# Performance work log

Measured on AMD Instinct MI355X. Metric: run time of the kernel, lower is better.

## Reference

```python
import jax, jax.numpy as jnp
import numpy as np

N_NODES = 50000
N_EDGES = 800000
NUM_RELATIONS = 8   # 2 * n_speakers**2 with n_speakers = 2
NUM_BASES = 30
G_DIM, H1_DIM, H2_DIM = 128, 128, 128


def setup_inputs() -> dict:
    key = jax.random.key(0)
    ks = jax.random.split(key, 10)
    inp = {
        "node_features": jax.random.normal(ks[0], (N_NODES, G_DIM), jnp.float32),
        "edge_index": jax.random.randint(ks[1], (2, N_EDGES), 0, N_NODES, dtype=jnp.int64),
        "edge_type": jax.random.randint(ks[2], (N_EDGES,), 0, NUM_RELATIONS, dtype=jnp.int64),
        "edge_norm": jax.random.uniform(ks[3], (N_EDGES,), jnp.float32),
        # RGCNConv params (basis decomposition)
        "basis": jax.random.normal(ks[4], (NUM_BASES, G_DIM, H1_DIM), jnp.float32) * 0.05,
        "comp": jax.random.normal(ks[5], (NUM_RELATIONS, NUM_BASES), jnp.float32) * 0.1,
        "root": jax.random.normal(ks[6], (G_DIM, H1_DIM), jnp.float32) * 0.05,
        "bias1": jnp.zeros((H1_DIM,), jnp.float32),
        # GraphConv params: lin_rel (with bias) applied to aggregated neighbors, lin_root (no bias)
        "w_rel": jax.random.normal(ks[7], (H1_DIM, H2_DIM), jnp.float32) * 0.05,
        "b_rel": jnp.zeros((H2_DIM,), jnp.float32),
        "w_root": jax.random.normal(ks[8], (H1_DIM, H2_DIM), jnp.float32) * 0.05,
    }
    return inp


def reference(node_features, edge_index, edge_type, edge_norm,
              basis, comp, root, bias1, w_rel, b_rel, w_root):
    src, dst = edge_index[0], edge_index[1]  # source_to_target flow (PyG default)

    # ---- Layer 1: RGCNConv with basis decomposition ----
    # W[r] = sum_b comp[r,b] * basis[b]  -> [R, g, h1]
    W = jnp.einsum('rb,bio->rio', comp, basis)
    # Project every node under every relation once (N*R*h1), then gather per edge.
    # Mathematically identical to per-edge x_j @ W[edge_type] but avoids an [E, g, h1] tensor.
    x_proj = jnp.einsum('ni,rio->nro', node_features, W)  # [N, R, h1]
    msg = x_proj[src, edge_type] * edge_norm[:, None]     # [E, h1]
    agg = jax.ops.segment_sum(msg, dst, num_segments=N_NODES)  # scatter-add to targets
    h = agg + node_features @ root + bias1                # [N, h1]

    # ---- Layer 2: GraphConv (aggr='add', no edge_weight) ----
    agg2 = jax.ops.segment_sum(h[src], dst, num_segments=N_NODES)  # [N, h1]
    out = agg2 @ w_rel + b_rel + h @ w_root               # [N, h2]
    return out
```

## Files before the change

kernel.cpp:

```cpp
#include <hip/hip_runtime.h>
#include <hip/hip_bf16.h>
#include <stdint.h>

#define N_NODES 50000
#define N_EDGES 800000
#define NREL    8
#define NBASES  30
#define DIM     128
#define NSLOT   9
#define NCAT    (NSLOT*DIM)
#define SCAN_NB ((N_NODES + 255) / 256)
#define NB_C    196
#define EPB_PLACE 2048
#define NBLK_PLACE ((N_EDGES + EPB_PLACE - 1) / EPB_PLACE)
#define GEMM1_TILES ((N_NODES + 63) / 64)
#define PREP_TOTAL  (NCAT * DIM + 2 * DIM * DIM)
#define PREP_BLKS   ((PREP_TOTAL + 255) / 256)
#define CONV_BLKS   ((N_NODES * DIM / 4 + 255) / 256)
#define HIST_BLKS   ((N_EDGES + 255) / 256)

typedef __attribute__((ext_vector_type(8))) short short8;
typedef __attribute__((ext_vector_type(4))) float floatx4;
typedef __hip_bfloat16  bf16;
typedef __hip_bfloat162 bf16x2;

__device__ inline ushort f2bu(float f) { bf16 b = __float2bfloat16(f); return *(ushort*)&b; }
__device__ inline float  bu2f(ushort u) { union { unsigned i; float f; } c; c.i = ((unsigned)u) << 16; return c.f; }

__global__ __launch_bounds__(256) void setup_kernel(const float* __restrict__ basis, const float* __restrict__ comp,
                                                    const float* __restrict__ root, const float* __restrict__ w_rel,
                                                    const float* __restrict__ w_root,
                                                    bf16* __restrict__ WcatT, bf16* __restrict__ wrelT,
                                                    bf16* __restrict__ wrootT,
                                                    const float4* __restrict__ x4, ushort4* __restrict__ xb4,
                                                    const int* __restrict__ ei, int* __restrict__ deg) {
    int b = blockIdx.x;
    if (b < PREP_BLKS) {
        int idx = b * 256 + threadIdx.x;
        const int n_cat = NCAT * DIM;
        const int n_sq  = DIM * DIM;
        if (idx < n_cat) {
            int k = idx & 127, n = idx >> 7;
            int r = n >> 7, o = n & 127;
            float v;
            if (r < NREL) {
                v = 0.f;
                for (int bb = 0; bb < NBASES; ++bb)
                    v += comp[r * NBASES + bb] * basis[(bb * DIM + k) * DIM + o];
            } else {
                v = root[k * DIM + o];
            }
            WcatT[n * DIM + k] = __float2bfloat16(v);
        } else if (idx < n_cat + n_sq) {
            int t = idx - n_cat; int k = t & 127, o = t >> 7;
            wrelT[o * DIM + k] = __float2bfloat16(w_rel[k * DIM + o]);
        } else if (idx < n_cat + 2 * n_sq) {
            int t = idx - n_cat - n_sq; int k = t & 127, o = t >> 7;
            wrootT[o * DIM + k] = __float2bfloat16(w_root[k * DIM + o]);
        }
    } else if (b < PREP_BLKS + CONV_BLKS) {
        int i = (b - PREP_BLKS) * 256 + threadIdx.x;
        int n4 = N_NODES * DIM / 4;
        if (i < n4) {
            float4 f = x4[i];
            ushort4 o;
            o.x = f2bu(f.x); o.y = f2bu(f.y); o.z = f2bu(f.z); o.w = f2bu(f.w);
            xb4[i] = o;
        }
    } else {
        int e = (b - PREP_BLKS - CONV_BLKS) * 256 + threadIdx.x;
        if (e < N_EDGES) atomicAdd(&deg[ei[N_EDGES + e]], 1);
    }
}

__global__ __launch_bounds__(256) void scan_one(const int* __restrict__ deg, int* __restrict__ segoff,
                                                unsigned long long* __restrict__ bstate, int n) {
    __shared__ int buf[256];
    int b = blockIdx.x, tid = threadIdx.x;
    int i = b * 256 + tid;
    int v = (i < n) ? deg[i] : 0;
    buf[tid] = v;
    __syncthreads();
#pragma unroll
    for (int o = 1; o < 256; o <<= 1) {
        int t = (tid >= o) ? buf[tid - o] : 0;
        __syncthreads();
        buf[tid] += t;
        __syncthreads();
    }
    int incl = buf[tid];
    int total = buf[255];
    if (tid == 0)
        __hip_atomic_store(&bstate[b], (1ULL << 32) | (unsigned)total,
                           __ATOMIC_RELEASE, __HIP_MEMORY_SCOPE_AGENT);
    int mysum = 0;
    for (int j = tid; j < b; j += 256) {
        unsigned long long s;
        do {
            s = __hip_atomic_load(&bstate[j], __ATOMIC_ACQUIRE, __HIP_MEMORY_SCOPE_AGENT);
        } while (!(s >> 32));
        mysum += (int)(s & 0xFFFFFFFFu);
    }
    __syncthreads();
    buf[tid] = mysum;
    __syncthreads();
#pragma unroll
    for (int o = 128; o > 0; o >>= 1) {
        if (tid < o) buf[tid] += buf[tid + o];
        __syncthreads();
    }
    int base = buf[0];
    if (i < n) segoff[i + 1] = base + incl;
    if (b == 0 && tid == 0) segoff[0] = 0;
}

__global__ __launch_bounds__(256) void gemm1_place(const bf16* __restrict__ A, const bf16* __restrict__ BT,
                                                   bf16* __restrict__ C, int M,
                                                   const int* __restrict__ ei, const int* __restrict__ et,
                                                   const float* __restrict__ en, const int* __restrict__ segoff,
                                                   int* __restrict__ bcur, uint2* __restrict__ tmp) {
    __shared__ ushort smem[2 * 64 * 136];
    int blk = blockIdx.x;
    if (blk < GEMM1_TILES) {
        ushort (*As)[136] = (ushort(*)[136])smem;
        ushort (*Bs)[136] = (ushort(*)[136])(smem + 64 * 136);
        const ushort* Au = (const ushort*)A;
        const ushort* Bu = (const ushort*)BT;
        ushort* Cu = (ushort*)C;
        int tm = blk * 64;
        int wave = threadIdx.x >> 6, lane = threadIdx.x & 63;
        int q = lane >> 4, mr = lane & 15;

#pragma unroll
        for (int u = 0; u < 4; ++u) {
            int cc = threadIdx.x + u * 256;
            int row = cc >> 4, seg = cc & 15;
            int gr = tm + row;
            short8 av = {0, 0, 0, 0, 0, 0, 0, 0};
            if (gr < M) av = *(const short8*)(Au + (size_t)gr * 128 + seg * 8);
            *(short8*)(&As[row][seg * 8]) = av;
        }

        floatx4 zero = {0.f, 0.f, 0.f, 0.f};
        for (int t = 0; t < 18; ++t) {
            if (t) __syncthreads();
#pragma unroll
            for (int u = 0; u < 4; ++u) {
                int cc = threadIdx.x + u * 256;
                int row = cc >> 4, seg = cc & 15;
                short8 bv = *(const short8*)(Bu + (size_t)(t * 64 + row) * 128 + seg * 8);
                *(short8*)(&Bs[row][seg * 8]) = bv;
            }
            __syncthreads();
            floatx4 acc[4] = {zero, zero, zero, zero};
#pragma unroll
            for (int kt = 0; kt < 4; ++kt) {
                short8 a = *(const short8*)(&As[wave * 16 + mr][q * 8 + kt * 32]);
#pragma unroll
                for (int nt = 0; nt < 4; ++nt) {
                    short8 bb = *(const short8*)(&Bs[nt * 16 + mr][q * 8 + kt * 32]);
                    acc[nt] = __builtin_amdgcn_mfma_f32_16x16x32_bf16(a, bb, acc[nt], 0, 0, 0);
                }
            }
#pragma unroll
            for (int nt = 0; nt < 4; ++nt)
#pragma unroll
                for (int r4 = 0; r4 < 4; ++r4) {
                    int row = tm + wave * 16 + q * 4 + r4;
                    if (row < M) Cu[(size_t)row * NCAT + t * 64 + nt * 16 + mr] = f2bu(acc[nt][r4]);
                }
        }
    } else {
        int* lhist = (int*)smem;
        int* lbase = lhist + NB_C;
        int* lrank = lbase + NB_C;
        int tid = threadIdx.x;
        for (int i = tid; i < NB_C; i += 256) { lhist[i] = 0; lrank[i] = 0; }
        __syncthreads();
        int e0 = (blk - GEMM1_TILES) * EPB_PLACE;
#pragma unroll
        for (int i = 0; i < EPB_PLACE / 256; ++i) {
            int e = e0 + i * 256 + tid;
            if (e < N_EDGES) atomicAdd(&lhist[ei[N_EDGES + e] >> 8], 1);
        }
        __syncthreads();
        for (int c = tid; c < NB_C; c += 256)
            if (lhist[c] > 0) lbase[c] = atomicAdd(&bcur[c], lhist[c]);
        __syncthreads();
#pragma unroll
        for (int i = 0; i < EPB_PLACE / 256; ++i) {
            int e = e0 + i * 256 + tid;
            if (e < N_EDGES) {
                int d = ei[N_EDGES + e];
                int c = d >> 8;
                int r = atomicAdd(&lrank[c], 1);
                int p = segoff[c << 8] + lbase[c] + r;
                tmp[p] = make_uint2((unsigned)ei[e] | ((unsigned)et[e] << 16) | ((unsigned)(d & 255) << 19),
                                    __float_as_uint(en[e]));
            }
        }
    }
}

__global__ __launch_bounds__(256) void sortb_kernel(const uint2* __restrict__ tmp, const int* __restrict__ segoff,
                                                    uint2* __restrict__ rec) {
    __shared__ int cur[256];
    int c = blockIdx.x;
    int tid = threadIdx.x;
    cur[tid] = 0;
    __syncthreads();
    int base = segoff[c << 8];
    int nlimit = (c + 1) << 8; if (nlimit > N_NODES) nlimit = N_NODES;
    int end = segoff[nlimit];
    for (int i = base + tid; i < end; i += 256) {
        uint2 r = tmp[i];
        int dl = (r.x >> 19) & 255;
        int p = segoff[(c << 8) + dl] + atomicAdd(&cur[dl], 1);
        rec[p] = make_uint2(r.x & 0x7FFFFu, r.y);
    }
}

__global__ void seg1_kernel(const uint2* __restrict__ rec, const int* __restrict__ segoff,
                            const ushort* __restrict__ proj, const float* __restrict__ bias1,
                            ushort* __restrict__ h) {
    int quad = threadIdx.x >> 4;
    int node = blockIdx.x * 16 + quad;
    if (node >= N_NODES) return;
    int lane = threadIdx.x & 15;
    int s = segoff[node], e = segoff[node + 1];
    float acc[8] = {0.f, 0.f, 0.f, 0.f, 0.f, 0.f, 0.f, 0.f};
    for (int chunk = s; chunk < e; chunk += 4) {
        int m = e - chunk; if (m > 4) m = 4;
        uint2 rr[4]; short8 vv[4];
#pragma unroll
        for (int j = 0; j < 4; ++j) if (j < m) rr[j] = rec[chunk + j];
#pragma unroll
        for (int j = 0; j < 4; ++j) if (j < m) {
            unsigned src = rr[j].x & 0xFFFFu;
            unsigned typ = rr[j].x >> 16;
            vv[j] = *(const short8*)(proj + ((size_t)src * NSLOT + typ) * 128 + lane * 8);
        }
#pragma unroll
        for (int j = 0; j < 4; ++j) if (j < m) {
            float norm = __uint_as_float(rr[j].y);
#pragma unroll
            for (int f = 0; f < 8; ++f) acc[f] += norm * bu2f((ushort)vv[j][f]);
        }
    }
    short8 base = *(const short8*)(proj + ((size_t)node * NSLOT + 8) * 128 + lane * 8);
    short8 o;
#pragma unroll
    for (int f = 0; f < 8; ++f)
        o[f] = (short)f2bu(acc[f] + bu2f((ushort)base[f]) + bias1[lane * 8 + f]);
    *(short8*)(h + (size_t)node * 128 + lane * 8) = o;
}

__global__ void seg2_kernel(const uint2* __restrict__ rec, const int* __restrict__ segoff,
                            const ushort* __restrict__ h, ushort* __restrict__ out2) {
    int quad = threadIdx.x >> 4;
    int node = blockIdx.x * 16 + quad;
    if (node >= N_NODES) return;
    int lane = threadIdx.x & 15;
    int s = segoff[node], e = segoff[node + 1];
    float acc[8] = {0.f, 0.f, 0.f, 0.f, 0.f, 0.f, 0.f, 0.f};
    for (int chunk = s; chunk < e; chunk += 4) {
        int m = e - chunk; if (m > 4) m = 4;
        uint2 rr[4]; short8 vv[4];
#pragma unroll
        for (int j = 0; j < 4; ++j) if (j < m) rr[j] = rec[chunk + j];
#pragma unroll
        for (int j = 0; j < 4; ++j) if (j < m)
            vv[j] = *(const short8*)(h + (size_t)(rr[j].x & 0xFFFFu) * 128 + lane * 8);
#pragma unroll
        for (int j = 0; j < 4; ++j) if (j < m)
#pragma unroll
            for (int f = 0; f < 8; ++f) acc[f] += bu2f((ushort)vv[j][f]);
    }
    short8 o;
#pragma unroll
    for (int f = 0; f < 8; ++f) o[f] = (short)f2bu(acc[f]);
    *(short8*)(out2 + (size_t)node * 128 + lane * 8) = o;
}

__global__ __launch_bounds__(256) void gemm2_kernel(const bf16* __restrict__ A1, const bf16* __restrict__ B1T,
                                                    const bf16* __restrict__ A2, const bf16* __restrict__ B2T,
                                                    const float* __restrict__ brel, float* __restrict__ out, int M) {
    __shared__ ushort As[64][136];
    __shared__ ushort Bs[64][136];
    int tm = blockIdx.x * 64, tn = blockIdx.y * 64;
    int wave = threadIdx.x >> 6, lane = threadIdx.x & 63;
    int q = lane >> 4, mr = lane & 15;
    floatx4 zero = {0.f, 0.f, 0.f, 0.f};
    floatx4 acc[4] = {zero, zero, zero, zero};

    for (int phase = 0; phase < 2; ++phase) {
        const ushort* Au = (const ushort*)(phase ? A2 : A1);
        const ushort* Bu = (const ushort*)(phase ? B2T : B1T);
        if (phase) __syncthreads();
        for (int c = threadIdx.x; c < 64 * 16; c += 256) {
            int row = c >> 4, seg = c & 15;
            int gr = tm + row;
            short8 av = {0, 0, 0, 0, 0, 0, 0, 0};
            if (gr < M) av = *(const short8*)(Au + (size_t)gr * 128 + seg * 8);
            *(short8*)(&As[row][seg * 8]) = av;
            short8 bv = *(const short8*)(Bu + (size_t)(tn + row) * 128 + seg * 8);
            *(short8*)(&Bs[row][seg * 8]) = bv;
        }
        __syncthreads();
#pragma unroll
        for (int kt = 0; kt < 4; ++kt) {
            short8 a = *(const short8*)(&As[wave * 16 + mr][q * 8 + kt * 32]);
#pragma unroll
            for (int nt = 0; nt < 4; ++nt) {
                short8 b = *(const short8*)(&Bs[nt * 16 + mr][q * 8 + kt * 32]);
                acc[nt] = __builtin_amdgcn_mfma_f32_16x16x32_bf16(a, b, acc[nt], 0, 0, 0);
            }
        }
    }
    __syncthreads();
    float* Csf = (float*)&As[0][0];
#pragma unroll
    for (int nt = 0; nt < 4; ++nt)
#pragma unroll
        for (int r4 = 0; r4 < 4; ++r4) {
            int row = wave * 16 + q * 4 + r4;
            int col = nt * 16 + mr;
            Csf[row * 68 + col] = acc[nt][r4] + brel[tn + col];
        }
    __syncthreads();
#pragma unroll
    for (int u = 0; u < 4; ++u) {
        int cc = threadIdx.x + u * 256;
        int row = cc >> 4, seg = cc & 15;
        int gr = tm + row;
        if (gr < M) {
            float4 v = *(const float4*)(&Csf[row * 68 + seg * 4]);
            *(float4*)(out + (size_t)gr * 128 + tn + seg * 4) = v;
        }
    }
}

extern "C" void kernel_launch(void* const* d_in, const int* in_sizes, int n_in,
                              void* d_out, int out_size, void* d_ws, size_t ws_size,
                              hipStream_t stream) {
    const float* x      = (const float*)d_in[0];
    const int*   ei     = (const int*)d_in[1];
    const int*   et     = (const int*)d_in[2];
    const float* en     = (const float*)d_in[3];
    const float* basis  = (const float*)d_in[4];
    const float* comp   = (const float*)d_in[5];
    const float* root   = (const float*)d_in[6];
    const float* bias1  = (const float*)d_in[7];
    const float* w_rel  = (const float*)d_in[8];
    const float* b_rel  = (const float*)d_in[9];
    const float* w_root = (const float*)d_in[10];
    float* out = (float*)d_out;

    char* ws = (char*)d_ws;
    size_t off = 0;
    auto alloc = [&](size_t bytes) { size_t o = off; off += (bytes + 255) & ~(size_t)255; return o; };

    size_t o_deg    = alloc((size_t)N_NODES * 4);
    size_t o_bcur   = alloc((size_t)NB_C * 4);
    size_t o_bstate = alloc((size_t)SCAN_NB * 8);
    size_t o_segoff = alloc((size_t)(N_NODES + 1) * 4);
    size_t o_rec    = alloc((size_t)N_EDGES * 8);
    size_t o_tmp    = alloc((size_t)N_EDGES * 8);
    size_t o_wcat   = alloc((size_t)NCAT * DIM * 2);
    size_t o_wrel   = alloc((size_t)DIM * DIM * 2);
    size_t o_wroot  = alloc((size_t)DIM * DIM * 2);
    size_t o_xb     = alloc((size_t)N_NODES * DIM * 2);
    size_t o_proj   = alloc((size_t)N_NODES * NCAT * 2);
    size_t o_hb     = alloc((size_t)N_NODES * DIM * 2);
    size_t o_agg2   = alloc((size_t)N_NODES * DIM * 2);

    int*   deg    = (int*)(ws + o_deg);
    int*   bcur   = (int*)(ws + o_bcur);
    unsigned long long* bstate = (unsigned long long*)(ws + o_bstate);
    int*   segoff = (int*)(ws + o_segoff);
    uint2* rec    = (uint2*)(ws + o_rec);
    uint2* tmp    = (uint2*)(ws + o_tmp);
    bf16*  wcat   = (bf16*)(ws + o_wcat);
    bf16*  wrelT  = (bf16*)(ws + o_wrel);
    bf16*  wrootT = (bf16*)(ws + o_wroot);
    bf16*  xb     = (bf16*)(ws + o_xb);
    bf16*  proj   = (bf16*)(ws + o_proj);
    bf16*  hb     = (bf16*)(ws + o_hb);
    bf16*  agg2   = (bf16*)(ws + o_agg2);

    hipMemsetAsync(ws + o_deg, 0, o_segoff - o_deg, stream);

    setup_kernel<<<PREP_BLKS + CONV_BLKS + HIST_BLKS, 256, 0, stream>>>(
        basis, comp, root, w_rel, w_root, wcat, wrelT, wrootT,
        (const float4*)x, (ushort4*)xb, ei, deg);
    scan_one<<<SCAN_NB, 256, 0, stream>>>(deg, segoff, bstate, N_NODES);
    gemm1_place<<<GEMM1_TILES + NBLK_PLACE, 256, 0, stream>>>(xb, wcat, proj, N_NODES,
                                                              ei, et, en, segoff, bcur, tmp);
    sortb_kernel<<<NB_C, 256, 0, stream>>>(tmp, segoff, rec);
    seg1_kernel<<<(N_NODES + 15) / 16, 256, 0, stream>>>(rec, segoff, (const ushort*)proj, bias1, (ushort*)hb);
    seg2_kernel<<<(N_NODES + 15) / 16, 256, 0, stream>>>(rec, segoff, (const ushort*)hb, (ushort*)agg2);
    {
        dim3 grid((N_NODES + 63) / 64, DIM / 64);
        gemm2_kernel<<<grid, 256, 0, stream>>>(agg2, wrelT, hb, wrootT, b_rel, out, N_NODES);
    }
}
```

Baseline: 320.8 us.

## Aggregate raw features per relation before projecting, replacing project-then-gather

Measured after the change: 350.5 us. 1.09x slower.

```diff
diff --git a/kernel.cpp b/kernel.cpp
--- a/kernel.cpp
+++ b/kernel.cpp
@@ -13,7 +13,7 @@
 #define NB_C    196
 #define EPB_PLACE 2048
 #define NBLK_PLACE ((N_EDGES + EPB_PLACE - 1) / EPB_PLACE)
-#define GEMM1_TILES ((N_NODES + 63) / 64)
+#define GEMMH_TILES ((N_NODES + 63) / 64)
 #define PREP_TOTAL  (NCAT * DIM + 2 * DIM * DIM)
 #define PREP_BLKS   ((PREP_TOTAL + 255) / 256)
 #define CONV_BLKS   ((N_NODES * DIM / 4 + 255) / 256)
@@ -30,7 +30,7 @@
 __global__ __launch_bounds__(256) void setup_kernel(const float* __restrict__ basis, const float* __restrict__ comp,
                                                     const float* __restrict__ root, const float* __restrict__ w_rel,
                                                     const float* __restrict__ w_root,
-                                                    bf16* __restrict__ WcatT, bf16* __restrict__ wrelT,
+                                                    bf16* __restrict__ W2T, bf16* __restrict__ wrelT,
                                                     bf16* __restrict__ wrootT,
                                                     const float4* __restrict__ x4, ushort4* __restrict__ xb4,
                                                     const int* __restrict__ ei, int* __restrict__ deg) {
@@ -40,8 +40,9 @@
         const int n_cat = NCAT * DIM;
         const int n_sq  = DIM * DIM;
         if (idx < n_cat) {
-            int k = idx & 127, n = idx >> 7;
-            int r = n >> 7, o = n & 127;
+            int o = idx / NCAT;
+            int rem = idx - o * NCAT;
+            int r = rem >> 7, k = rem & 127;
             float v;
             if (r < NREL) {
                 v = 0.f;
@@ -50,7 +51,7 @@
             } else {
                 v = root[k * DIM + o];
             }
-            WcatT[n * DIM + k] = __float2bfloat16(v);
+            W2T[idx] = __float2bfloat16(v);
         } else if (idx < n_cat + n_sq) {
             int t = idx - n_cat; int k = t & 127, o = t >> 7;
             wrelT[o * DIM + k] = __float2bfloat16(w_rel[k * DIM + o]);
@@ -114,145 +115,174 @@
     if (b == 0 && tid == 0) segoff[0] = 0;
 }
 
-__global__ __launch_bounds__(256) void gemm1_place(const bf16* __restrict__ A, const bf16* __restrict__ BT,
-                                                   bf16* __restrict__ C, int M,
-                                                   const int* __restrict__ ei, const int* __restrict__ et,
-                                                   const float* __restrict__ en, const int* __restrict__ segoff,
-                                                   int* __restrict__ bcur, uint2* __restrict__ tmp) {
-    __shared__ ushort smem[2 * 64 * 136];
-    int blk = blockIdx.x;
-    if (blk < GEMM1_TILES) {
-        ushort (*As)[136] = (ushort(*)[136])smem;
-        ushort (*Bs)[136] = (ushort(*)[136])(smem + 64 * 136);
-        const ushort* Au = (const ushort*)A;
-        const ushort* Bu = (const ushort*)BT;
-        ushort* Cu = (ushort*)C;
-        int tm = blk * 64;
-        int wave = threadIdx.x >> 6, lane = threadIdx.x & 63;
-        int q = lane >> 4, mr = lane & 15;
-
+__global__ __launch_bounds__(256) void place_kernel(const int* __restrict__ ei, const int* __restrict__ et,
+                                                    const float* __restrict__ en, const int* __restrict__ segoff,
+                                                    int* __restrict__ bcur, uint2* __restrict__ tmp) {
+    __shared__ int lhist[NB_C];
+    __shared__ int lbase[NB_C];
+    __shared__ int lrank[NB_C];
+    int tid = threadIdx.x;
+    for (int i = tid; i < NB_C; i += 256) { lhist[i] = 0; lrank[i] = 0; }
+    __syncthreads();
+    int e0 = blockIdx.x * EPB_PLACE;
+#pragma unroll
+    for (int i = 0; i < EPB_PLACE / 256; ++i) {
+        int e = e0 + i * 256 + tid;
+        if (e < N_EDGES) atomicAdd(&lhist[ei[N_EDGES + e] >> 8], 1);
+    }
+    __syncthreads();
+    for (int c = tid; c < NB_C; c += 256)
+        if (lhist[c] > 0) lbase[c] = atomicAdd(&bcur[c], lhist[c]);
+    __syncthreads();
+#pragma unroll
+    for (int i = 0; i < EPB_PLACE / 256; ++i) {
+        int e = e0 + i * 256 + tid;
+        if (e < N_EDGES) {
+            int d = ei[N_EDGES + e];
+            int c = d >> 8;
+            int r = atomicAdd(&lrank[c], 1);
+            int p = segoff[c << 8] + lbase[c] + r;
+            tmp[p] = make_uint2((unsigned)ei[e] | ((unsigned)et[e] << 16) | ((unsigned)(d & 255) << 19),
+                                __float_as_uint(en[e]));
+        }
+    }
+}
+
+__global__ __launch_bounds__(256) void sortb_kernel(const uint2* __restrict__ tmp, const int* __restrict__ segoff,
+                                                    uint2* __restrict__ rec) {
+    __shared__ int hist2[256 * 8];
+    int c = blockIdx.x;
+    int tid = threadIdx.x;
+    for (int i = tid; i < 256 * 8; i += 256) hist2[i] = 0;
+    __syncthreads();
+    int base = segoff[c << 8];
+    int nlimit = (c + 1) << 8; if (nlimit > N_NODES) nlimit = N_NODES;
+    int end = segoff[nlimit];
+    for (int i = base + tid; i < end; i += 256) {
+        unsigned x = tmp[i].x;
+        int dl = (x >> 19) & 255, ty = (x >> 16) & 7;
+        atomicAdd(&hist2[dl * 8 + ty], 1);
+    }
+    __syncthreads();
+    {
+        int node = (c << 8) + tid;
+        int run = (node < N_NODES) ? (segoff[node] - base) : 0;
+#pragma unroll
+        for (int t = 0; t < 8; ++t) {
+            int cnt = hist2[tid * 8 + t];
+            hist2[tid * 8 + t] = run;
+            run += cnt;
+        }
+    }
+    __syncthreads();
+    for (int i = base + tid; i < end; i += 256) {
+        uint2 r = tmp[i];
+        int dl = (r.x >> 19) & 255, ty = (r.x >> 16) & 7;
+        int p = base + atomicAdd(&hist2[dl * 8 + ty], 1);
+        rec[p] = make_uint2(r.x & 0x7FFFFu, r.y);
+    }
+}
+
+__device__ inline void flush8(ushort* dst, const float* acc) {
+    short8 o;
+#pragma unroll
+    for (int f = 0; f < 8; ++f) o[f] = (short)f2bu(acc[f]);
+    *(short8*)dst = o;
+}
+
+__global__ void gath1_kernel(const uint2* __restrict__ rec, const int* __restrict__ segoff,
+                             const ushort* __restrict__ xb, ushort* __restrict__ s) {
+    int quad = threadIdx.x >> 4;
+    int node = blockIdx.x * 16 + quad;
+    if (node >= N_NODES) return;
+    int lane = threadIdx.x & 15;
+    ushort* sp = s + (size_t)node * NCAT + lane * 8;
+    int st = segoff[node], en = segoff[node + 1];
+    float acc[8] = {0.f, 0.f, 0.f, 0.f, 0.f, 0.f, 0.f, 0.f};
+    int cur = -1;
+    unsigned mask = 0;
+    for (int chunk = st; chunk < en; chunk += 4) {
+        int m = en - chunk; if (m > 4) m = 4;
+        uint2 rr[4]; short8 vv[4];
+#pragma unroll
+        for (int j = 0; j < 4; ++j) if (j < m) rr[j] = rec[chunk + j];
+#pragma unroll
+        for (int j = 0; j < 4; ++j) if (j < m)
+            vv[j] = *(const short8*)(xb + (size_t)(rr[j].x & 0xFFFFu) * 128 + lane * 8);
+#pragma unroll
+        for (int j = 0; j < 4; ++j) if (j < m) {
+            int ty = (int)(rr[j].x >> 16);
+            if (ty != cur) {
+                if (cur >= 0) flush8(sp + cur * 128, acc);
+                cur = ty;
+                mask |= 1u << ty;
+#pragma unroll
+                for (int f = 0; f < 8; ++f) acc[f] = 0.f;
+            }
+            float nrm = __uint_as_float(rr[j].y);
+#pragma unroll
+            for (int f = 0; f < 8; ++f) acc[f] += nrm * bu2f((ushort)vv[j][f]);
+        }
+    }
+    if (cur >= 0) flush8(sp + cur * 128, acc);
+    short8 z = {0, 0, 0, 0, 0, 0, 0, 0};
+#pragma unroll
+    for (int t = 0; t < 8; ++t)
+        if (!(mask & (1u << t))) *(short8*)(sp + t * 128) = z;
+    *(short8*)(sp + 8 * 128) = *(const short8*)(xb + (size_t)node * 128 + lane * 8);
+}
+
+__global__ __launch_bounds__(256) void gemmh_kernel(const bf16* __restrict__ S, const bf16* __restrict__ B2T,
+                                                    const float* __restrict__ bias1, bf16* __restrict__ H, int M) {
+    __shared__ ushort As[64][136];
+    __shared__ ushort Bs[128][136];
+    const ushort* Su = (const ushort*)S;
+    const ushort* Bu = (const ushort*)B2T;
+    ushort* Hu = (ushort*)H;
+    int tm = blockIdx.x * 64;
+    int wave = threadIdx.x >> 6, lane = threadIdx.x & 63;
+    int q = lane >> 4, mr = lane & 15;
+    floatx4 zero = {0.f, 0.f, 0.f, 0.f};
+    floatx4 acc[8] = {zero, zero, zero, zero, zero, zero, zero, zero};
+
+    for (int ch = 0; ch < 9; ++ch) {
+        if (ch) __syncthreads();
 #pragma unroll
         for (int u = 0; u < 4; ++u) {
             int cc = threadIdx.x + u * 256;
             int row = cc >> 4, seg = cc & 15;
             int gr = tm + row;
             short8 av = {0, 0, 0, 0, 0, 0, 0, 0};
-            if (gr < M) av = *(const short8*)(Au + (size_t)gr * 128 + seg * 8);
+            if (gr < M) av = *(const short8*)(Su + (size_t)gr * NCAT + ch * 128 + seg * 8);
             *(short8*)(&As[row][seg * 8]) = av;
         }
-
-        floatx4 zero = {0.f, 0.f, 0.f, 0.f};
-        for (int t = 0; t < 18; ++t) {
-            if (t) __syncthreads();
-#pragma unroll
-            for (int u = 0; u < 4; ++u) {
-                int cc = threadIdx.x + u * 256;
-                int row = cc >> 4, seg = cc & 15;
-                short8 bv = *(const short8*)(Bu + (size_t)(t * 64 + row) * 128 + seg * 8);
-                *(short8*)(&Bs[row][seg * 8]) = bv;
+#pragma unroll
+        for (int u = 0; u < 8; ++u) {
+            int cc = threadIdx.x + u * 256;
+            int row = cc >> 4, seg = cc & 15;
+            short8 bv = *(const short8*)(Bu + (size_t)row * NCAT + ch * 128 + seg * 8);
+            *(short8*)(&Bs[row][seg * 8]) = bv;
+        }
+        __syncthreads();
+#pragma unroll
+        for (int kt = 0; kt < 4; ++kt) {
+            short8 a = *(const short8*)(&As[wave * 16 + mr][q * 8 + kt * 32]);
+#pragma unroll
+            for (int nt = 0; nt < 8; ++nt) {
+                short8 b = *(const short8*)(&Bs[nt * 16 + mr][q * 8 + kt * 32]);
+                acc[nt] = __builtin_amdgcn_mfma_f32_16x16x32_bf16(a, b, acc[nt], 0, 0, 0);
             }
-            __syncthreads();
-            floatx4 acc[4] = {zero, zero, zero, zero};
-#pragma unroll
-            for (int kt = 0; kt < 4; ++kt) {
-                short8 a = *(const short8*)(&As[wave * 16 + mr][q * 8 + kt * 32]);
-#pragma unroll
-                for (int nt = 0; nt < 4; ++nt) {
-                    short8 bb = *(const short8*)(&Bs[nt * 16 + mr][q * 8 + kt * 32]);
-                    acc[nt] = __builtin_amdgcn_mfma_f32_16x16x32_bf16(a, bb, acc[nt], 0, 0, 0);
-                }
-            }
-#pragma unroll
-            for (int nt = 0; nt < 4; ++nt)
-#pragma unroll
-                for (int r4 = 0; r4 < 4; ++r4) {
-                    int row = tm + wave * 16 + q * 4 + r4;
-                    if (row < M) Cu[(size_t)row * NCAT + t * 64 + nt * 16 + mr] = f2bu(acc[nt][r4]);
-                }
-        }
-    } else {
-        int* lhist = (int*)smem;
-        int* lbase = lhist + NB_C;
-        int* lrank = lbase + NB_C;
-        int tid = threadIdx.x;
-        for (int i = tid; i < NB_C; i += 256) { lhist[i] = 0; lrank[i] = 0; }
-        __syncthreads();
-        int e0 = (blk - GEMM1_TILES) * EPB_PLACE;
-#pragma unroll
-        for (int i = 0; i < EPB_PLACE / 256; ++i) {
-            int e = e0 + i * 256 + tid;
-            if (e < N_EDGES) atomicAdd(&lhist[ei[N_EDGES + e] >> 8], 1);
-        }
-        __syncthreads();
-        for (int c = tid; c < NB_C; c += 256)
-            if (lhist[c] > 0) lbase[c] = atomicAdd(&bcur[c], lhist[c]);
-        __syncthreads();
-#pragma unroll
-        for (int i = 0; i < EPB_PLACE / 256; ++i) {
-            int e = e0 + i * 256 + tid;
-            if (e < N_EDGES) {
-                int d = ei[N_EDGES + e];
-                int c = d >> 8;
-                int r = atomicAdd(&lrank[c], 1);
-                int p = segoff[c << 8] + lbase[c] + r;
-                tmp[p] = make_uint2((unsigned)ei[e] | ((unsigned)et[e] << 16) | ((unsigned)(d & 255) << 19),
-                                    __float_as_uint(en[e]));
-            }
-        }
-    }
-}
-
-__global__ __launch_bounds__(256) void sortb_kernel(const uint2* __restrict__ tmp, const int* __restrict__ segoff,
-                                                    uint2* __restrict__ rec) {
-    __shared__ int cur[256];
-    int c = blockIdx.x;
-    int tid = threadIdx.x;
-    cur[tid] = 0;
-    __syncthreads();
-    int base = segoff[c << 8];
-    int nlimit = (c + 1) << 8; if (nlimit > N_NODES) nlimit = N_NODES;
-    int end = segoff[nlimit];
-    for (int i = base + tid; i < end; i += 256) {
-        uint2 r = tmp[i];
-        int dl = (r.x >> 19) & 255;
-        int p = segoff[(c << 8) + dl] + atomicAdd(&cur[dl], 1);
-        rec[p] = make_uint2(r.x & 0x7FFFFu, r.y);
-    }
-}
-
-__global__ void seg1_kernel(const uint2* __restrict__ rec, const int* __restrict__ segoff,
-                            const ushort* __restrict__ proj, const float* __restrict__ bias1,
-                            ushort* __restrict__ h) {
-    int quad = threadIdx.x >> 4;
-    int node = blockIdx.x * 16 + quad;
-    if (node >= N_NODES) return;
-    int lane = threadIdx.x & 15;
-    int s = segoff[node], e = segoff[node + 1];
-    float acc[8] = {0.f, 0.f, 0.f, 0.f, 0.f, 0.f, 0.f, 0.f};
-    for (int chunk = s; chunk < e; chunk += 4) {
-        int m = e - chunk; if (m > 4) m = 4;
-        uint2 rr[4]; short8 vv[4];
-#pragma unroll
-        for (int j = 0; j < 4; ++j) if (j < m) rr[j] = rec[chunk + j];
-#pragma unroll
-        for (int j = 0; j < 4; ++j) if (j < m) {
-            unsigned src = rr[j].x & 0xFFFFu;
-            unsigned typ = rr[j].x >> 16;
-            vv[j] = *(const short8*)(proj + ((size_t)src * NSLOT + typ) * 128 + lane * 8);
-        }
-#pragma unroll
-        for (int j = 0; j < 4; ++j) if (j < m) {
-            float norm = __uint_as_float(rr[j].y);
-#pragma unroll
-            for (int f = 0; f < 8; ++f) acc[f] += norm * bu2f((ushort)vv[j][f]);
-        }
-    }
-    short8 base = *(const short8*)(proj + ((size_t)node * NSLOT + 8) * 128 + lane * 8);
-    short8 o;
-#pragma unroll
-    for (int f = 0; f < 8; ++f)
-        o[f] = (short)f2bu(acc[f] + bu2f((ushort)base[f]) + bias1[lane * 8 + f]);
-    *(short8*)(h + (size_t)node * 128 + lane * 8) = o;
+        }
+    }
+#pragma unroll
+    for (int nt = 0; nt < 8; ++nt) {
+        float bi = bias1[nt * 16 + mr];
+#pragma unroll
+        for (int r4 = 0; r4 < 4; ++r4) {
+            int row = tm + wave * 16 + q * 4 + r4;
+            if (row < M) Hu[(size_t)row * 128 + nt * 16 + mr] = f2bu(acc[nt][r4] + bi);
+        }
+    }
 }
 
 __global__ void seg2_kernel(const uint2* __restrict__ rec, const int* __restrict__ segoff,
@@ -261,10 +291,10 @@
     int node = blockIdx.x * 16 + quad;
     if (node >= N_NODES) return;
     int lane = threadIdx.x & 15;
-    int s = segoff[node], e = segoff[node + 1];
+    int st = segoff[node], en = segoff[node + 1];
     float acc[8] = {0.f, 0.f, 0.f, 0.f, 0.f, 0.f, 0.f, 0.f};
-    for (int chunk = s; chunk < e; chunk += 4) {
-        int m = e - chunk; if (m > 4) m = 4;
+    for (int chunk = st; chunk < en; chunk += 4) {
+        int m = en - chunk; if (m > 4) m = 4;
         uint2 rr[4]; short8 vv[4];
 #pragma unroll
         for (int j = 0; j < 4; ++j) if (j < m) rr[j] = rec[chunk + j];
@@ -366,11 +396,11 @@
     size_t o_segoff = alloc((size_t)(N_NODES + 1) * 4);
     size_t o_rec    = alloc((size_t)N_EDGES * 8);
     size_t o_tmp    = alloc((size_t)N_EDGES * 8);
-    size_t o_wcat   = alloc((size_t)NCAT * DIM * 2);
+    size_t o_w2t    = alloc((size_t)NCAT * DIM * 2);
     size_t o_wrel   = alloc((size_t)DIM * DIM * 2);
     size_t o_wroot  = alloc((size_t)DIM * DIM * 2);
     size_t o_xb     = alloc((size_t)N_NODES * DIM * 2);
-    size_t o_proj   = alloc((size_t)N_NODES * NCAT * 2);
+    size_t o_s      = alloc((size_t)N_NODES * NCAT * 2);
     size_t o_hb     = alloc((size_t)N_NODES * DIM * 2);
     size_t o_agg2   = alloc((size_t)N_NODES * DIM * 2);
 
@@ -380,24 +410,24 @@
     int*   segoff = (int*)(ws + o_segoff);
     uint2* rec    = (uint2*)(ws + o_rec);
     uint2* tmp    = (uint2*)(ws + o_tmp);
-    bf16*  wcat   = (bf16*)(ws + o_wcat);
+    bf16*  w2t    = (bf16*)(ws + o_w2t);
     bf16*  wrelT  = (bf16*)(ws + o_wrel);
     bf16*  wrootT = (bf16*)(ws + o_wroot);
     bf16*  xb     = (bf16*)(ws + o_xb);
-    bf16*  proj   = (bf16*)(ws + o_proj);
+    bf16*  sbuf   = (bf16*)(ws + o_s);
     bf16*  hb     = (bf16*)(ws + o_hb);
     bf16*  agg2   = (bf16*)(ws + o_agg2);
 
     hipMemsetAsync(ws + o_deg, 0, o_segoff - o_deg, stream);
 
     setup_kernel<<<PREP_BLKS + CONV_BLKS + HIST_BLKS, 256, 0, stream>>>(
-        basis, comp, root, w_rel, w_root, wcat, wrelT, wrootT,
+        basis, comp, root, w_rel, w_root, w2t, wrelT, wrootT,
         (const float4*)x, (ushort4*)xb, ei, deg);
     scan_one<<<SCAN_NB, 256, 0, stream>>>(deg, segoff, bstate, N_NODES);
-    gemm1_place<<<GEMM1_TILES + NBLK_PLACE, 256, 0, stream>>>(xb, wcat, proj, N_NODES,
-                                                              ei, et, en, segoff, bcur, tmp);
+    place_kernel<<<NBLK_PLACE, 256, 0, stream>>>(ei, et, en, segoff, bcur, tmp);
     sortb_kernel<<<NB_C, 256, 0, stream>>>(tmp, segoff, rec);
-    seg1_kernel<<<(N_NODES + 15) / 16, 256, 0, stream>>>(rec, segoff, (const ushort*)proj, bias1, (ushort*)hb);
+    gath1_kernel<<<(N_NODES + 15) / 16, 256, 0, stream>>>(rec, segoff, (const ushort*)xb, (ushort*)sbuf);
+    gemmh_kernel<<<GEMMH_TILES, 256, 0, stream>>>(sbuf, w2t, bias1, hb, N_NODES);
     seg2_kernel<<<(N_NODES + 15) / 16, 256, 0, stream>>>(rec, segoff, (const ushort*)hb, (ushort*)agg2);
     {
         dim3 grid((N_NODES + 63) / 64, DIM / 64);
```
